# Kernel tuning notes

Measured on AMD Instinct MI355X. Metric: run time of the kernel, lower is better.

Reference implementation:

```python
import jax, jax.numpy as jnp
import numpy as np

TAU = 0.08


def setup_inputs() -> dict:
    key = jax.random.key(0)
    k1, k2 = jax.random.split(key)
    pos_waves = jax.random.normal(k1, (32, 64, 8192), dtype=jnp.float32)
    neg_waves = jax.random.normal(k2, (32, 64, 8192), dtype=jnp.float32)
    return {"pos_waves": pos_waves, "neg_waves": neg_waves}


def _normalize(w):
    # global min/max over the whole wave tensor (matches torch.min/torch.max on 2D tensor)
    lo = jnp.min(w, axis=(1, 2), keepdims=True)  # [N,1,1]
    hi = jnp.max(w, axis=(1, 2), keepdims=True)
    return (w - lo) / (hi - lo)


def _pairwise_negpearson(X, Y):
    # X: [N,B,T], Y: [M,B,T] -> mean over B of (1 - pearson) for every (n,m) pair
    T = X.shape[-1]
    sx = jnp.sum(X, axis=-1)            # [N,B]
    sy = jnp.sum(Y, axis=-1)            # [M,B]
    sx2 = jnp.sum(X * X, axis=-1)       # [N,B]
    sy2 = jnp.sum(Y * Y, axis=-1)       # [M,B]
    sxy = jnp.einsum('nbt,mbt->nmb', X, Y)  # [N,M,B]
    num = T * sxy - sx[:, None, :] * sy[None, :, :]
    den = jnp.sqrt((T * sx2 - sx * sx)[:, None, :] * (T * sy2 - sy * sy)[None, :, :])
    return jnp.mean(1.0 - num / den, axis=-1)  # [N,M]


def reference(pos_waves, neg_waves):
    P = _normalize(pos_waves)   # [N,B,T]
    Q = _normalize(neg_waves)   # [M,B,T]
    N = P.shape[0]

    d_pp = _pairwise_negpearson(P, P)                    # [N,N]
    upper = jnp.triu(jnp.ones((N, N), dtype=bool), k=1)  # i < j pairs only
    pos_total = jnp.sum(jnp.where(upper, jnp.exp(d_pp / TAU), 0.0))

    d_pn = _pairwise_negpearson(P, Q)                    # [N,M]
    neg_total = jnp.sum(jnp.exp(d_pn / TAU))

    return jnp.log10(pos_total / neg_total + 1.0)
```

## Files before the change

### kernel.cpp

```cpp
#include <hip/hip_runtime.h>
#include <cmath>

#define N_ 32
#define B_ 64
#define T_ 8192
#define CPB 16
#define PSTRIDE 2176
#define PADH 264

typedef _Float16 half4 __attribute__((ext_vector_type(4)));
typedef _Float16 half8 __attribute__((ext_vector_type(8)));
typedef float floatx4 __attribute__((ext_vector_type(4)));

__global__ __launch_bounds__(512, 8) void k_stage1(const float* __restrict__ pos,
                                                   const float* __restrict__ neg,
                                                   float* __restrict__ partial) {
    __shared__ _Float16 tile[2][32][PADH];

    const int bid = blockIdx.x;
    const int b = bid >> 4, c = bid & 15;
    const int tid = threadIdx.x;
    const int wave = tid >> 6, lane = tid & 63;
    const int row = tid >> 4;
    const int idx = tid & 15;
    const int mat = wave >> 2;
    const int qi = (wave >> 1) & 1, qj = wave & 1;
    const int m16 = lane & 15, h2 = lane >> 4;

    const float* xrow = pos + ((long)row * B_ + b) * T_ + c * 512;
    const float* yrow = neg + ((long)row * B_ + b) * T_ + c * 512;

    floatx4 acc = {};
    float sx = 0.f, sx2 = 0.f, sy = 0.f, sy2 = 0.f;

#pragma unroll
    for (int s = 0; s < 2; ++s) {
        __syncthreads();
        const float4* px = (const float4*)(xrow + s * 256);
        const float4* py = (const float4*)(yrow + s * 256);

        float4 vx[4], vy[4];
#pragma unroll
        for (int f = 0; f < 4; ++f) vx[f] = px[f * 16 + idx];
#pragma unroll
        for (int f = 0; f < 4; ++f) vy[f] = py[f * 16 + idx];
#pragma unroll
        for (int f = 0; f < 4; ++f) {
            float4 v = vx[f];
            sx += v.x + v.y + v.z + v.w;
            sx2 = fmaf(v.x, v.x, sx2); sx2 = fmaf(v.y, v.y, sx2);
            sx2 = fmaf(v.z, v.z, sx2); sx2 = fmaf(v.w, v.w, sx2);
            half4 hv = {(_Float16)v.x, (_Float16)v.y, (_Float16)v.z, (_Float16)v.w};
            *(half4*)&tile[0][row][(f * 16 + idx) * 4] = hv;
        }
#pragma unroll
        for (int f = 0; f < 4; ++f) {
            float4 u = vy[f];
            sy += u.x + u.y + u.z + u.w;
            sy2 = fmaf(u.x, u.x, sy2); sy2 = fmaf(u.y, u.y, sy2);
            sy2 = fmaf(u.z, u.z, sy2); sy2 = fmaf(u.w, u.w, sy2);
            half4 hu = {(_Float16)u.x, (_Float16)u.y, (_Float16)u.z, (_Float16)u.w};
            *(half4*)&tile[1][row][(f * 16 + idx) * 4] = hu;
        }
        __syncthreads();

        const _Float16* abase = &tile[0][qi * 16 + m16][h2 * 8];
        const _Float16* bbase = &tile[mat][qj * 16 + m16][h2 * 8];
#pragma unroll
        for (int k = 0; k < 8; ++k) {
            half8 af = *(const half8*)(abase + k * 32);
            half8 bf = *(const half8*)(bbase + k * 32);
            acc = __builtin_amdgcn_mfma_f32_16x16x32_f16(af, bf, acc, 0, 0, 0);
        }
    }

    sx += __shfl_xor(sx, 1); sx += __shfl_xor(sx, 2);
    sx += __shfl_xor(sx, 4); sx += __shfl_xor(sx, 8);
    sx2 += __shfl_xor(sx2, 1); sx2 += __shfl_xor(sx2, 2);
    sx2 += __shfl_xor(sx2, 4); sx2 += __shfl_xor(sx2, 8);
    sy += __shfl_xor(sy, 1); sy += __shfl_xor(sy, 2);
    sy += __shfl_xor(sy, 4); sy += __shfl_xor(sy, 8);
    sy2 += __shfl_xor(sy2, 1); sy2 += __shfl_xor(sy2, 2);
    sy2 += __shfl_xor(sy2, 4); sy2 += __shfl_xor(sy2, 8);

    float* out = partial + (long)bid * PSTRIDE;
    if ((tid & 15) < 4) {
        int kind = tid & 3;
        float v = (kind == 0) ? sx : (kind == 1) ? sx2 : (kind == 2) ? sy : sy2;
        out[2048 + kind * 32 + row] = v;
    }

#pragma unroll
    for (int reg = 0; reg < 4; ++reg) {
        int rr = qi * 16 + h2 * 4 + reg;
        int cc = qj * 16 + m16;
        out[mat * 1024 + rr * 32 + cc] = acc[reg];
    }
}

__global__ void k_reduce(const float* __restrict__ partial, float* __restrict__ red) {
    const int b = blockIdx.y;
    const int o = blockIdx.x * 128 + threadIdx.x;
    const float* in = partial + (long)b * CPB * PSTRIDE;
    float s = 0.f;
#pragma unroll
    for (int c = 0; c < CPB; ++c) s += in[c * PSTRIDE + o];
    red[(long)b * PSTRIDE + o] = s;
}

__global__ void k_entries(const float* __restrict__ red, double* __restrict__ blocksums) {
    const int tid = threadIdx.x;
    const int w = tid >> 6, lane = tid & 63;
    const int entry = blockIdx.x * 4 + w;
    const int mat = entry >> 10;
    const int idx = entry & 1023;
    const int n = idx >> 5, m = idx & 31;

    const float* rb = red + (long)lane * PSTRIDE;
    float g = rb[mat * 1024 + idx];
    float sxn = rb[2048 + n];
    float sx2n = rb[2080 + n];
    float sym, sy2m;
    if (mat == 0) {
        sym = rb[2048 + m];
        sy2m = rb[2080 + m];
    } else {
        sym = rb[2112 + m];
        sy2m = rb[2144 + m];
    }

    double num = (double)T_ * (double)g - (double)sxn * (double)sym;
    double vx = (double)T_ * (double)sx2n - (double)sxn * (double)sxn;
    double vy = (double)T_ * (double)sy2m - (double)sym * (double)sym;
    double contrib = 1.0 - num / sqrt(vx * vy);

#pragma unroll
    for (int off = 32; off; off >>= 1) contrib += __shfl_down(contrib, off);

    __shared__ double s_pos[4], s_neg[4];
    if (lane == 0) {
        double d = contrib * (1.0 / B_);
        double term = exp(d / 0.08);
        double p = 0.0, q = 0.0;
        if (mat == 0) {
            if (n < m) p = term;
        } else {
            q = term;
        }
        s_pos[w] = p;
        s_neg[w] = q;
    }
    __syncthreads();
    if (tid == 0) {
        blocksums[blockIdx.x * 2 + 0] = s_pos[0] + s_pos[1] + s_pos[2] + s_pos[3];
        blocksums[blockIdx.x * 2 + 1] = s_neg[0] + s_neg[1] + s_neg[2] + s_neg[3];
    }
}

__global__ void k_final(const double* __restrict__ blocksums, float* __restrict__ out) {
    __shared__ double sp[256], sn[256];
    const int tid = threadIdx.x;
    double p = 0.0, q = 0.0;
    for (int i = tid; i < 512; i += 256) {
        p += blocksums[2 * i + 0];
        q += blocksums[2 * i + 1];
    }
    sp[tid] = p;
    sn[tid] = q;
    __syncthreads();
    for (int s = 128; s; s >>= 1) {
        if (tid < s) {
            sp[tid] += sp[tid + s];
            sn[tid] += sn[tid + s];
        }
        __syncthreads();
    }
    if (tid == 0) out[0] = (float)log10(sp[0] / sn[0] + 1.0);
}

extern "C" void kernel_launch(void* const* d_in, const int* in_sizes, int n_in,
                              void* d_out, int out_size, void* d_ws, size_t ws_size,
                              hipStream_t stream) {
    const float* pos = (const float*)d_in[0];
    const float* neg = (const float*)d_in[1];
    float* out = (float*)d_out;

    char* ws = (char*)d_ws;
    float* partial = (float*)ws;
    float* red = (float*)(ws + (size_t)1024 * PSTRIDE * 4);
    double* blocksums = (double*)(ws + (size_t)1024 * PSTRIDE * 4 + (size_t)64 * PSTRIDE * 4);

    k_stage1<<<1024, 512, 0, stream>>>(pos, neg, partial);
    k_reduce<<<dim3(17, 64), 128, 0, stream>>>(partial, red);
    k_entries<<<512, 256, 0, stream>>>(red, blocksums);
    k_final<<<1, 256, 0, stream>>>(blocksums, out);
}
```

Measured before the change: 153.5 us.

## Load MFMA fragments directly from global, fuse reduction stages, use atomic finalization

Stage 1 now loads fp32 rows straight into registers in MFMA fragment layout, with 4 waves each covering a 128-wide T slice. It computes the symmetric PP tiles (skipping one) and all PN tiles without an LDS staging tile, then reduces across waves in shared memory and writes a transposed partial buffer. The separate reduce and final kernels are removed: k_entries sums the 16 chunk partials itself and finishes with double atomics plus a last-block counter. This cuts launches, LDS traffic and redundant lower-triangle MFMA work, at the cost of serialized per-wave LDS accumulation and strided transposed stores.

```diff
diff --git a/kernel.cpp b/kernel.cpp
--- a/kernel.cpp
+++ b/kernel.cpp
@@ -4,111 +4,114 @@
 #define N_ 32
 #define B_ 64
 #define T_ 8192
-#define CPB 16
-#define PSTRIDE 2176
-#define PADH 264
+#define NBLK1 1024
+#define PS 2176
 
-typedef _Float16 half4 __attribute__((ext_vector_type(4)));
 typedef _Float16 half8 __attribute__((ext_vector_type(8)));
 typedef float floatx4 __attribute__((ext_vector_type(4)));
 
-__global__ __launch_bounds__(512, 8) void k_stage1(const float* __restrict__ pos,
-                                                   const float* __restrict__ neg,
-                                                   float* __restrict__ partial) {
-    __shared__ _Float16 tile[2][32][PADH];
+__device__ __forceinline__ half8 cvt8(const float4 v0, const float4 v1,
+                                      float& s, float& s2) {
+    s += v0.x + v0.y + v0.z + v0.w + v1.x + v1.y + v1.z + v1.w;
+    s2 = fmaf(v0.x, v0.x, s2); s2 = fmaf(v0.y, v0.y, s2);
+    s2 = fmaf(v0.z, v0.z, s2); s2 = fmaf(v0.w, v0.w, s2);
+    s2 = fmaf(v1.x, v1.x, s2); s2 = fmaf(v1.y, v1.y, s2);
+    s2 = fmaf(v1.z, v1.z, s2); s2 = fmaf(v1.w, v1.w, s2);
+    half8 r = {(_Float16)v0.x, (_Float16)v0.y, (_Float16)v0.z, (_Float16)v0.w,
+               (_Float16)v1.x, (_Float16)v1.y, (_Float16)v1.z, (_Float16)v1.w};
+    return r;
+}
 
+__global__ __launch_bounds__(256, 2)
+void k_stage1(const float* __restrict__ pos, const float* __restrict__ neg,
+              float* __restrict__ pt, double* __restrict__ accs,
+              unsigned* __restrict__ ctr) {
+    __shared__ float red_s[PS];
     const int bid = blockIdx.x;
-    const int b = bid >> 4, c = bid & 15;
+    const int b = bid & 63, cg = bid >> 6;
     const int tid = threadIdx.x;
-    const int wave = tid >> 6, lane = tid & 63;
-    const int row = tid >> 4;
-    const int idx = tid & 15;
-    const int mat = wave >> 2;
-    const int qi = (wave >> 1) & 1, qj = wave & 1;
-    const int m16 = lane & 15, h2 = lane >> 4;
+    const int w = tid >> 6, lane = tid & 63;
+    const int m = lane & 15, h = lane >> 4;
 
-    const float* xrow = pos + ((long)row * B_ + b) * T_ + c * 512;
-    const float* yrow = neg + ((long)row * B_ + b) * T_ + c * 512;
+    if (bid == 0 && tid == 0) { accs[0] = 0.0; accs[1] = 0.0; *ctr = 0u; }
 
-    floatx4 acc = {};
-    float sx = 0.f, sx2 = 0.f, sy = 0.f, sy2 = 0.f;
+    const long tb = (long)cg * 512 + w * 128 + h * 8;
+    const float4* pa0 = (const float4*)(pos + ((long)m * B_ + b) * T_ + tb);
+    const float4* pa1 = (const float4*)(pos + ((long)(m + 16) * B_ + b) * T_ + tb);
+    const float4* pb0 = (const float4*)(neg + ((long)m * B_ + b) * T_ + tb);
+    const float4* pb1 = (const float4*)(neg + ((long)(m + 16) * B_ + b) * T_ + tb);
+
+    float4 a0[4][2], a1[4][2], b0[4][2], b1[4][2];
+#pragma unroll
+    for (int kk = 0; kk < 4; ++kk) {
+        a0[kk][0] = pa0[kk * 8]; a0[kk][1] = pa0[kk * 8 + 1];
+        a1[kk][0] = pa1[kk * 8]; a1[kk][1] = pa1[kk * 8 + 1];
+        b0[kk][0] = pb0[kk * 8]; b0[kk][1] = pb0[kk * 8 + 1];
+        b1[kk][0] = pb1[kk * 8]; b1[kk][1] = pb1[kk * 8 + 1];
+    }
+
+    floatx4 cPP00 = {}, cPP01 = {}, cPP11 = {};
+    floatx4 cPN00 = {}, cPN01 = {}, cPN10 = {}, cPN11 = {};
+    float sxl = 0.f, sxl2 = 0.f, sxh = 0.f, sxh2 = 0.f;
+    float syl = 0.f, syl2 = 0.f, syh = 0.f, syh2 = 0.f;
 
 #pragma unroll
-    for (int s = 0; s < 2; ++s) {
-        __syncthreads();
-        const float4* px = (const float4*)(xrow + s * 256);
-        const float4* py = (const float4*)(yrow + s * 256);
+    for (int kk = 0; kk < 4; ++kk) {
+        half8 fa0 = cvt8(a0[kk][0], a0[kk][1], sxl, sxl2);
+        half8 fa1 = cvt8(a1[kk][0], a1[kk][1], sxh, sxh2);
+        half8 fb0 = cvt8(b0[kk][0], b0[kk][1], syl, syl2);
+        half8 fb1 = cvt8(b1[kk][0], b1[kk][1], syh, syh2);
+        cPP00 = __builtin_amdgcn_mfma_f32_16x16x32_f16(fa0, fa0, cPP00, 0, 0, 0);
+        cPP01 = __builtin_amdgcn_mfma_f32_16x16x32_f16(fa0, fa1, cPP01, 0, 0, 0);
+        cPP11 = __builtin_amdgcn_mfma_f32_16x16x32_f16(fa1, fa1, cPP11, 0, 0, 0);
+        cPN00 = __builtin_amdgcn_mfma_f32_16x16x32_f16(fa0, fb0, cPN00, 0, 0, 0);
+        cPN01 = __builtin_amdgcn_mfma_f32_16x16x32_f16(fa0, fb1, cPN01, 0, 0, 0);
+        cPN10 = __builtin_amdgcn_mfma_f32_16x16x32_f16(fa1, fb0, cPN10, 0, 0, 0);
+        cPN11 = __builtin_amdgcn_mfma_f32_16x16x32_f16(fa1, fb1, cPN11, 0, 0, 0);
+    }
 
-        float4 vx[4], vy[4];
+    sxl += __shfl_xor(sxl, 16);   sxl += __shfl_xor(sxl, 32);
+    sxl2 += __shfl_xor(sxl2, 16); sxl2 += __shfl_xor(sxl2, 32);
+    sxh += __shfl_xor(sxh, 16);   sxh += __shfl_xor(sxh, 32);
+    sxh2 += __shfl_xor(sxh2, 16); sxh2 += __shfl_xor(sxh2, 32);
+    syl += __shfl_xor(syl, 16);   syl += __shfl_xor(syl, 32);
+    syl2 += __shfl_xor(syl2, 16); syl2 += __shfl_xor(syl2, 32);
+    syh += __shfl_xor(syh, 16);   syh += __shfl_xor(syh, 32);
+    syh2 += __shfl_xor(syh2, 16); syh2 += __shfl_xor(syh2, 32);
+
+    for (int i = tid; i < PS; i += 256) red_s[i] = 0.f;
+    __syncthreads();
 #pragma unroll
-        for (int f = 0; f < 4; ++f) vx[f] = px[f * 16 + idx];
+    for (int wv = 0; wv < 4; ++wv) {
+        if (w == wv) {
 #pragma unroll
-        for (int f = 0; f < 4; ++f) vy[f] = py[f * 16 + idx];
-#pragma unroll
-        for (int f = 0; f < 4; ++f) {
-            float4 v = vx[f];
-            sx += v.x + v.y + v.z + v.w;
-            sx2 = fmaf(v.x, v.x, sx2); sx2 = fmaf(v.y, v.y, sx2);
-            sx2 = fmaf(v.z, v.z, sx2); sx2 = fmaf(v.w, v.w, sx2);
-            half4 hv = {(_Float16)v.x, (_Float16)v.y, (_Float16)v.z, (_Float16)v.w};
-            *(half4*)&tile[0][row][(f * 16 + idx) * 4] = hv;
-        }
-#pragma unroll
-        for (int f = 0; f < 4; ++f) {
-            float4 u = vy[f];
-            sy += u.x + u.y + u.z + u.w;
-            sy2 = fmaf(u.x, u.x, sy2); sy2 = fmaf(u.y, u.y, sy2);
-            sy2 = fmaf(u.z, u.z, sy2); sy2 = fmaf(u.w, u.w, sy2);
-            half4 hu = {(_Float16)u.x, (_Float16)u.y, (_Float16)u.z, (_Float16)u.w};
-            *(half4*)&tile[1][row][(f * 16 + idx) * 4] = hu;
+            for (int reg = 0; reg < 4; ++reg) {
+                const int r = h * 4 + reg;
+                red_s[r * 32 + m]                    += cPP00[reg];
+                red_s[r * 32 + 16 + m]               += cPP01[reg];
+                red_s[(16 + r) * 32 + 16 + m]        += cPP11[reg];
+                red_s[1024 + r * 32 + m]             += cPN00[reg];
+                red_s[1024 + r * 32 + 16 + m]        += cPN01[reg];
+                red_s[1024 + (16 + r) * 32 + m]      += cPN10[reg];
+                red_s[1024 + (16 + r) * 32 + 16 + m] += cPN11[reg];
+            }
+            const int row = (h & 1) * 16 + m;
+            const int base = 2048 + (h >> 1) * 64;
+            const float s1 = (h == 0) ? sxl : (h == 1) ? sxh : (h == 2) ? syl : syh;
+            const float s2 = (h == 0) ? sxl2 : (h == 1) ? sxh2 : (h == 2) ? syl2 : syh2;
+            red_s[base + row] += s1;
+            red_s[base + 32 + row] += s2;
         }
         __syncthreads();
-
-        const _Float16* abase = &tile[0][qi * 16 + m16][h2 * 8];
-        const _Float16* bbase = &tile[mat][qj * 16 + m16][h2 * 8];
-#pragma unroll
-        for (int k = 0; k < 8; ++k) {
-            half8 af = *(const half8*)(abase + k * 32);
-            half8 bf = *(const half8*)(bbase + k * 32);
-            acc = __builtin_amdgcn_mfma_f32_16x16x32_f16(af, bf, acc, 0, 0, 0);
-        }
     }
 
-    sx += __shfl_xor(sx, 1); sx += __shfl_xor(sx, 2);
-    sx += __shfl_xor(sx, 4); sx += __shfl_xor(sx, 8);
-    sx2 += __shfl_xor(sx2, 1); sx2 += __shfl_xor(sx2, 2);
-    sx2 += __shfl_xor(sx2, 4); sx2 += __shfl_xor(sx2, 8);
-    sy += __shfl_xor(sy, 1); sy += __shfl_xor(sy, 2);
-    sy += __shfl_xor(sy, 4); sy += __shfl_xor(sy, 8);
-    sy2 += __shfl_xor(sy2, 1); sy2 += __shfl_xor(sy2, 2);
-    sy2 += __shfl_xor(sy2, 4); sy2 += __shfl_xor(sy2, 8);
-
-    float* out = partial + (long)bid * PSTRIDE;
-    if ((tid & 15) < 4) {
-        int kind = tid & 3;
-        float v = (kind == 0) ? sx : (kind == 1) ? sx2 : (kind == 2) ? sy : sy2;
-        out[2048 + kind * 32 + row] = v;
-    }
-
-#pragma unroll
-    for (int reg = 0; reg < 4; ++reg) {
-        int rr = qi * 16 + h2 * 4 + reg;
-        int cc = qj * 16 + m16;
-        out[mat * 1024 + rr * 32 + cc] = acc[reg];
-    }
+    for (int i = tid; i < PS; i += 256)
+        pt[(long)i * NBLK1 + bid] = red_s[i];
 }
 
-__global__ void k_reduce(const float* __restrict__ partial, float* __restrict__ red) {
-    const int b = blockIdx.y;
-    const int o = blockIdx.x * 128 + threadIdx.x;
-    const float* in = partial + (long)b * CPB * PSTRIDE;
-    float s = 0.f;
-#pragma unroll
-    for (int c = 0; c < CPB; ++c) s += in[c * PSTRIDE + o];
-    red[(long)b * PSTRIDE + o] = s;
-}
-
-__global__ void k_entries(const float* __restrict__ red, double* __restrict__ blocksums) {
+__global__ __launch_bounds__(256)
+void k_entries(const float* __restrict__ pt, double* __restrict__ accs,
+               unsigned* __restrict__ ctr, float* __restrict__ out) {
     const int tid = threadIdx.x;
     const int w = tid >> 6, lane = tid & 63;
     const int entry = blockIdx.x * 4 + w;
@@ -116,18 +119,19 @@
     const int idx = entry & 1023;
     const int n = idx >> 5, m = idx & 31;
 
-    const float* rb = red + (long)lane * PSTRIDE;
-    float g = rb[mat * 1024 + idx];
-    float sxn = rb[2048 + n];
-    float sx2n = rb[2080 + n];
-    float sym, sy2m;
-    if (mat == 0) {
-        sym = rb[2048 + m];
-        sy2m = rb[2080 + m];
-    } else {
-        sym = rb[2112 + m];
-        sy2m = rb[2144 + m];
-    }
+    auto rowsum = [&](int o) -> float {
+        const float* p = pt + (long)o * NBLK1 + lane;
+        float s = 0.f;
+#pragma unroll
+        for (int c = 0; c < 16; ++c) s += p[c * 64];
+        return s;
+    };
+
+    const float g    = rowsum(mat * 1024 + idx);
+    const float sxn  = rowsum(2048 + n);
+    const float sx2n = rowsum(2080 + n);
+    const float sym  = rowsum(mat ? 2112 + m : 2048 + m);
+    const float sy2m = rowsum(mat ? 2144 + m : 2080 + m);
 
     double num = (double)T_ * (double)g - (double)sxn * (double)sym;
     double vx = (double)T_ * (double)sx2n - (double)sxn * (double)sxn;
@@ -142,56 +146,38 @@
         double d = contrib * (1.0 / B_);
         double term = exp(d / 0.08);
         double p = 0.0, q = 0.0;
-        if (mat == 0) {
-            if (n < m) p = term;
-        } else {
-            q = term;
-        }
-        s_pos[w] = p;
-        s_neg[w] = q;
+        if (mat == 0) { if (n < m) p = term; }
+        else q = term;
+        s_pos[w] = p; s_neg[w] = q;
     }
     __syncthreads();
     if (tid == 0) {
-        blocksums[blockIdx.x * 2 + 0] = s_pos[0] + s_pos[1] + s_pos[2] + s_pos[3];
-        blocksums[blockIdx.x * 2 + 1] = s_neg[0] + s_neg[1] + s_neg[2] + s_neg[3];
+        atomicAdd(&accs[0], s_pos[0] + s_pos[1] + s_pos[2] + s_pos[3]);
+        atomicAdd(&accs[1], s_neg[0] + s_neg[1] + s_neg[2] + s_neg[3]);
+        __threadfence();
+        const unsigned old = atomicAdd(ctr, 1u);
+        if (old == gridDim.x - 1) {
+            __threadfence();
+            const double p = ((volatile double*)accs)[0];
+            const double q = ((volatile double*)accs)[1];
+            out[0] = (float)log10(p / q + 1.0);
+        }
     }
-}
-
-__global__ void k_final(const double* __restrict__ blocksums, float* __restrict__ out) {
-    __shared__ double sp[256], sn[256];
-    const int tid = threadIdx.x;
-    double p = 0.0, q = 0.0;
-    for (int i = tid; i < 512; i += 256) {
-        p += blocksums[2 * i + 0];
-        q += blocksums[2 * i + 1];
-    }
-    sp[tid] = p;
-    sn[tid] = q;
-    __syncthreads();
-    for (int s = 128; s; s >>= 1) {
-        if (tid < s) {
-            sp[tid] += sp[tid + s];
-            sn[tid] += sn[tid + s];
-        }
-        __syncthreads();
-    }
-    if (tid == 0) out[0] = (float)log10(sp[0] / sn[0] + 1.0);
 }
 
 extern "C" void kernel_launch(void* const* d_in, const int* in_sizes, int n_in,
                               void* d_out, int out_size, void* d_ws, size_t ws_size,
                               hipStream_t stream) {
+    (void)in_sizes; (void)n_in; (void)out_size; (void)ws_size;
     const float* pos = (const float*)d_in[0];
     const float* neg = (const float*)d_in[1];
     float* out = (float*)d_out;
 
     char* ws = (char*)d_ws;
-    float* partial = (float*)ws;
-    float* red = (float*)(ws + (size_t)1024 * PSTRIDE * 4);
-    double* blocksums = (double*)(ws + (size_t)1024 * PSTRIDE * 4 + (size_t)64 * PSTRIDE * 4);
+    float* pt = (float*)ws;
+    double* accs = (double*)(ws + (size_t)PS * NBLK1 * 4);
+    unsigned* ctr = (unsigned*)(ws + (size_t)PS * NBLK1 * 4 + 16);
 
-    k_stage1<<<1024, 512, 0, stream>>>(pos, neg, partial);
-    k_reduce<<<dim3(17, 64), 128, 0, stream>>>(partial, red);
-    k_entries<<<512, 256, 0, stream>>>(red, blocksums);
-    k_final<<<1, 256, 0, stream>>>(blocksums, out);
+    k_stage1<<<NBLK1, 256, 0, stream>>>(pos, neg, pt, accs, ctr);
+    k_entries<<<512, 256, 0, stream>>>(pt, accs, ctr, out);
 }
```

After: 189.6 us. 23.5% more time.
